# Kernel optimization log

Hardware: AMD Instinct MI355X
Metric: run time of the kernel (lower is better)

Reference implementation:

```python
import jax, jax.numpy as jnp
import numpy as np

B, T_D, T_P = 64, 256, 1024
DRUG_DIM, PROT_DIM, D = 128, 128, 128
MAX_LEN = 1024
NEG = -1e9


def _linear_params(k, out_d, in_d):
    k1, k2 = jax.random.split(k)
    lim = 1.0 / np.sqrt(in_d)
    W = jax.random.uniform(k1, (out_d, in_d), minval=-lim, maxval=lim, dtype=jnp.float32)
    b = jax.random.uniform(k2, (out_d,), minval=-lim, maxval=lim, dtype=jnp.float32)
    return W, b


def setup_inputs() -> dict:
    key = jax.random.key(0)
    ks = jax.random.split(key, 13)
    inp = {
        'smiles_embeddings': jax.random.normal(ks[0], (B, T_D, DRUG_DIM), dtype=jnp.float32),
        'protein_embeddings': jax.random.normal(ks[1], (B, T_P, PROT_DIM), dtype=jnp.float32),
        'smiles_mask': jax.random.randint(ks[2], (B, T_D), 0, 2, dtype=jnp.int32),
        'protein_mask': jax.random.randint(ks[3], (B, T_P), 0, 2, dtype=jnp.int32),
        # torch inits pos_bias to zeros; small random values make the test nontrivial
        'pos_bias': 0.02 * jax.random.normal(ks[4], (MAX_LEN, MAX_LEN), dtype=jnp.float32),
    }
    names = [('Wqd', 'bqd', DRUG_DIM), ('Wkp', 'bkp', PROT_DIM), ('Wvp', 'bvp', PROT_DIM),
             ('Wqp', 'bqp', PROT_DIM), ('Wkd', 'bkd', DRUG_DIM), ('Wvd', 'bvd', DRUG_DIM),
             ('Wpd', 'bpd', D), ('Wpp', 'bpp', D)]
    for i, (wn, bn, in_d) in enumerate(names):
        W, b = _linear_params(ks[5 + i], D, in_d)
        inp[wn] = W
        inp[bn] = b
    return inp


def _lin(x, W, b):
    return x @ W.T + b


def _aft(q, k, v, pb_masked, Wp, bp):
    # q: [B,Ti,D]; k,v: [B,Tj,D]; pb_masked: [B,Ti,Tj]
    max_k = k.max(axis=1, keepdims=True)              # per (b,d) over seq j
    max_pb = pb_masked.max(axis=2, keepdims=True)     # per (b,i) over j
    exp_k = jnp.exp(k - max_k)                        # [B,Tj,D]
    exp_pb = jnp.exp(pb_masked - max_pb)              # [B,Ti,Tj]
    num = jnp.einsum('bij,bjd->bid', exp_pb, exp_k * v)
    den = jnp.einsum('bij,bjd->bid', exp_pb, exp_k)
    y = jax.nn.sigmoid(q) * num / den
    return _lin(y, Wp, bp)


def reference(smiles_embeddings, protein_embeddings, smiles_mask, protein_mask, pos_bias,
              Wqd, bqd, Wkp, bkp, Wvp, bvp, Wqp, bqp, Wkd, bkd, Wvd, bvd, Wpd, bpd, Wpp, bpp):
    Td = smiles_embeddings.shape[1]
    Tp = protein_embeddings.shape[1]
    combined = smiles_mask[:, :, None] * protein_mask[:, None, :]  # [B,Td,Tp]
    pb = pos_bias[:Td, :Tp][None]                                   # [1,Td,Tp]

    # drug queries attend over protein keys/values
    pb_d = jnp.where(combined == 0, NEG, pb)
    y_d = _aft(_lin(smiles_embeddings, Wqd, bqd),
               _lin(protein_embeddings, Wkp, bkp),
               _lin(protein_embeddings, Wvp, bvp), pb_d, Wpd, bpd)

    # protein queries attend over drug keys/values (transposed pos bias)
    pb_p = jnp.where(jnp.swapaxes(combined, 1, 2) == 0, NEG, jnp.swapaxes(pb, 1, 2))
    y_p = _aft(_lin(protein_embeddings, Wqp, bqp),
               _lin(smiles_embeddings, Wkd, bkd),
               _lin(smiles_embeddings, Wvd, bvd), pb_p, Wpp, bpp)

    y_d = jnp.where(smiles_mask[:, :, None] == 0, NEG, y_d).max(axis=1)   # [B,D]
    y_p = jnp.where(protein_mask[:, :, None] == 0, NEG, y_p).max(axis=1)  # [B,D]
    return y_d, y_p
```

## Files before the change

### kernel.cpp

```cpp
#include <hip/hip_runtime.h>
#include <cstdint>
#include <cstddef>

#define NEGV -1e9f

typedef __bf16 bf16x8 __attribute__((ext_vector_type(8)));
typedef float f32x4 __attribute__((ext_vector_type(4)));
typedef unsigned short us4 __attribute__((ext_vector_type(4)));
typedef unsigned short us8 __attribute__((ext_vector_type(8)));

__device__ __forceinline__ unsigned short f2bf(float f) {
  unsigned int u = __float_as_uint(f);
  u += 0x7fffu + ((u >> 16) & 1u);
  return (unsigned short)(u >> 16);
}
__device__ __forceinline__ float bf2f(unsigned short u) {
  return __uint_as_float(((unsigned)u) << 16);
}


__global__ void prep_kernel(const float* __restrict__ w0, const float* __restrict__ w1,
                            const float* __restrict__ w2, const float* __restrict__ w3,
                            const float* __restrict__ w4, const float* __restrict__ w5,
                            const float* __restrict__ w6, const float* __restrict__ w7,
                            unsigned short* __restrict__ Wbf,
                            const float* __restrict__ pb,
                            unsigned short* __restrict__ epb,
                            unsigned short* __restrict__ epbT,
                            unsigned int* __restrict__ outEnc) {
  __shared__ unsigned short t[32][33];
  const int blk = blockIdx.x, tid = threadIdx.x;
  if (blk < 64) {
    outEnc[blk * 256 + tid] = 0u;
    return;
  }
  if (blk < 192) {
    const float* Ws[8] = {w0, w1, w2, w3, w4, w5, w6, w7};
    int idx = (blk - 64) * 256 + tid;
    int mat = idx >> 12, off = idx & 4095;
    float4 v = *(const float4*)&Ws[mat][(size_t)off * 4];
    us4 p;
    p.x = f2bf(v.x); p.y = f2bf(v.y); p.z = f2bf(v.z); p.w = f2bf(v.w);
    *(us4*)&Wbf[(size_t)mat * 16384 + (size_t)off * 4] = p;
    return;
  }
  const int bid = blk - 192;
  const int j0 = (bid & 31) * 32, i0 = (bid >> 5) * 32;
  const int tx = tid & 31, ty = tid >> 5;
#pragma unroll
  for (int r = 0; r < 4; ++r) {
    int i = i0 + ty + r * 8;
    unsigned short u = f2bf(__expf(pb[(size_t)i * 1024 + j0 + tx]));
    epb[(size_t)i * 1024 + j0 + tx] = u;
    t[ty + r * 8][tx] = u;
  }
  __syncthreads();
#pragma unroll
  for (int r = 0; r < 4; ++r)
    epbT[(size_t)(j0 + ty + r * 8) * 256 + i0 + tx] = t[tx][ty + r * 8];
}

__global__ __launch_bounds__(512, 4) void proj3_all(
    const float* __restrict__ smiles, const float* __restrict__ prot,
    const int* __restrict__ smask, const int* __restrict__ pmask,
    const unsigned short* __restrict__ Wbf,
    const float* __restrict__ bqd, const float* __restrict__ bkd, const float* __restrict__ bvd,
    const float* __restrict__ bqp, const float* __restrict__ bkp, const float* __restrict__ bvp,
    const unsigned short* __restrict__ epb, const unsigned short* __restrict__ epbT,
    unsigned short* __restrict__ AFd, unsigned short* __restrict__ AFp,
    unsigned short* __restrict__ SQd, unsigned short* __restrict__ BKd,
    unsigned short* __restrict__ BVd,
    unsigned short* __restrict__ SQp, unsigned short* __restrict__ BKp,
    unsigned short* __restrict__ BVp) {
  const int tid = threadIdx.x;

  if (blockIdx.x >= 1280) {
    int sid = (blockIdx.x - 1280) * 512 + tid;
    if (sid < 32768) {
      int lane = sid & 63, kt = (sid >> 6) & 31, it = sid >> 11;
      int i = it * 16 + (lane & 15), j = kt * 32 + (lane >> 4) * 8;
      *(us8*)&AFd[(size_t)sid * 8] = *(const us8*)&epb[(size_t)i * 1024 + j];
    } else {
      int s2 = sid - 32768;
      int lane = s2 & 63, kt = (s2 >> 6) & 7, it = s2 >> 9;
      int i = it * 16 + (lane & 15), j = kt * 32 + (lane >> 4) * 8;
      *(us8*)&AFp[(size_t)s2 * 8] = *(const us8*)&epbT[(size_t)i * 256 + j];
    }
    return;
  }

  __shared__ unsigned short xL[64 * 136];

  const float* X; const int* mask;
  const unsigned short *Wq, *Wk, *Wv;
  const float *bq, *bk_, *bv;
  unsigned short *SQ, *BK, *BV;
  int T, g0;
  if (blockIdx.x < 256) {
    X = smiles; mask = smask; T = 256; g0 = blockIdx.x * 64;
    Wq = Wbf; Wk = Wbf + 16384; Wv = Wbf + 32768;
    bq = bqd; bk_ = bkd; bv = bvd;
    SQ = SQd; BK = BKd; BV = BVd;
  } else {
    X = prot; mask = pmask; T = 1024; g0 = (blockIdx.x - 256) * 64;
    Wq = Wbf + 3 * 16384; Wk = Wbf + 4 * 16384; Wv = Wbf + 5 * 16384;
    bq = bqp; bk_ = bkp; bv = bvp;
    SQ = SQp; BK = BKp; BV = BVp;
  }
  const int b = g0 / T;
  const int tl0 = g0 - b * T;
  const int NIT = T / 16, NKT = T / 32;

#pragma unroll
  for (int r = 0; r < 4; ++r) {
    int i4 = tid + 512 * r;
    int t = i4 >> 5, k4 = (i4 & 31) * 4;
    float4 v = *(const float4*)&X[(size_t)(g0 + t) * 128 + k4];
    us4 p;
    p.x = f2bf(v.x); p.y = f2bf(v.y); p.z = f2bf(v.z); p.w = f2bf(v.w);
    *(us4*)&xL[t * 136 + k4] = p;
  }
  __syncthreads();

  const int lane = tid & 63, wave = tid >> 6;
  const int lo = lane & 15, hi = lane >> 4;

  if (wave < 4) {
    const int d0 = wave * 32;
    f32x4 aK[4][2], aV[4][2];
#pragma unroll
    for (int a = 0; a < 4; ++a)
#pragma unroll
      for (int s = 0; s < 2; ++s)
#pragma unroll
        for (int r = 0; r < 4; ++r) { aK[a][s][r] = 0.f; aV[a][s][r] = 0.f; }

#pragma unroll
    for (int kt = 0; kt < 128; kt += 32) {
      bf16x8 bK[2], bV[2];
#pragma unroll
      for (int s = 0; s < 2; ++s) {
        size_t roff = (size_t)(d0 + s * 16 + lo) * 128 + kt + hi * 8;
        bK[s] = *(const bf16x8*)&Wk[roff];
        bV[s] = *(const bf16x8*)&Wv[roff];
      }
#pragma unroll
      for (int a = 0; a < 4; ++a) {
        bf16x8 af = *(const bf16x8*)&xL[(a * 16 + lo) * 136 + kt + hi * 8];
#pragma unroll
        for (int s = 0; s < 2; ++s) {
          aK[a][s] = __builtin_amdgcn_mfma_f32_16x16x32_bf16(af, bK[s], aK[a][s], 0, 0, 0);
          aV[a][s] = __builtin_amdgcn_mfma_f32_16x16x32_bf16(af, bV[s], aV[a][s], 0, 0, 0);
        }
      }
    }

#pragma unroll
    for (int s = 0; s < 2; ++s) {
      int dt = (d0 >> 4) + s;
      float bbk = bk_[d0 + s * 16 + lo], bbv = bv[d0 + s * 16 + lo];
#pragma unroll
      for (int a = 0; a < 4; ++a) {
        int kt = (tl0 >> 5) + (a >> 1);
        int lane_f = ((a & 1) * 2 + (hi >> 1)) * 16 + lo;
        us4 vk, vv;
#pragma unroll
        for (int r = 0; r < 4; ++r) {
          int tg = g0 + a * 16 + hi * 4 + r;
          int mk = mask[tg];
          float ek = mk ? __expf(aK[a][s][r] + bbk) : 0.f;
          float ekv = ek * (aV[a][s][r] + bbv);
          vk[r] = f2bf(ek);
          vv[r] = f2bf(ekv);
        }
        size_t q4 = ((((size_t)b * NKT + kt) * 8 + dt) * 64 + lane_f) * 2 + (hi & 1);
        ((us4*)BK)[q4] = vk;
        ((us4*)BV)[q4] = vv;
      }
    }
  } else {
    const int d0 = (wave - 4) * 32;
    f32x4 aQ[4][2];
#pragma unroll
    for (int a = 0; a < 4; ++a)
#pragma unroll
      for (int s = 0; s < 2; ++s)
#pragma unroll
        for (int r = 0; r < 4; ++r) aQ[a][s][r] = 0.f;

#pragma unroll
    for (int kt = 0; kt < 128; kt += 32) {
      bf16x8 bQ[2];
#pragma unroll
      for (int s = 0; s < 2; ++s) {
        size_t roff = (size_t)(d0 + s * 16 + lo) * 128 + kt + hi * 8;
        bQ[s] = *(const bf16x8*)&Wq[roff];
      }
#pragma unroll
      for (int a = 0; a < 4; ++a) {
        bf16x8 af = *(const bf16x8*)&xL[(a * 16 + lo) * 136 + kt + hi * 8];
#pragma unroll
        for (int s = 0; s < 2; ++s)
          aQ[a][s] = __builtin_amdgcn_mfma_f32_16x16x32_bf16(af, bQ[s], aQ[a][s], 0, 0, 0);
      }
    }

#pragma unroll
    for (int s = 0; s < 2; ++s) {
      int dt = (d0 >> 4) + s;
      float bb = bq[d0 + s * 16 + lo];
#pragma unroll
      for (int a = 0; a < 4; ++a) {
        int it = (tl0 >> 4) + a;
        us4 v;
#pragma unroll
        for (int r = 0; r < 4; ++r) {
          float q = aQ[a][s][r] + bb;
          v[r] = f2bf(1.f / (1.f + __expf(-q)));
        }
        ((us4*)SQ)[(((size_t)b * NIT + it) * 8 + dt) * 64 + lane] = v;
      }
    }
  }
}

__global__ __launch_bounds__(512, 4) void aft_all(
    const unsigned short* __restrict__ AFd, const unsigned short* __restrict__ AFp,
    const unsigned short* __restrict__ SQd, const unsigned short* __restrict__ BKd,
    const unsigned short* __restrict__ BVd,
    const unsigned short* __restrict__ SQp, const unsigned short* __restrict__ BKp,
    const unsigned short* __restrict__ BVp,
    const int* __restrict__ smask, const int* __restrict__ pmask,
    const unsigned short* __restrict__ Wbf,
    const float* __restrict__ bpd, const float* __restrict__ bpp,
    unsigned int* __restrict__ outEnc) {
  __shared__ unsigned short smem[16384 + 128 * 136];
  unsigned short* denL = smem;
  unsigned short* yL = smem + 16384;

  const int blk = blockIdx.x;
  const unsigned short *AF, *BK, *BV, *SQ, *Wp;
  const float* bp;
  const int* msk;
  unsigned int* oEnc;
  int b, i0, NKT, NIT;
  if (blk < 128) {
    b = blk & 63; i0 = (blk >> 6) * 128; NKT = 32; NIT = 16;
    AF = AFd; BK = BKp; BV = BVp; SQ = SQd;
    Wp = Wbf + 6 * 16384; bp = bpd; msk = smask + b * 256 + i0; oEnc = outEnc;
  } else {
    int k = blk - 128;
    b = k & 63; i0 = (k >> 6) * 128; NKT = 8; NIT = 64;
    AF = AFp; BK = BKd; BV = BVd; SQ = SQp;
    Wp = Wbf + 7 * 16384; bp = bpp; msk = pmask + b * 1024 + i0; oEnc = outEnc + 8192;
  }

  const int tid = threadIdx.x, lane = tid & 63, w = tid >> 6;
  const int lo = lane & 15, hi = lane >> 4;
  const int wv = w & 3;
  const int wi = (wv >> 1) * 64, wd = (wv & 1) * 64;
  const int it0 = (i0 + wi) >> 4;
  const int dt0 = wd >> 4;

  const unsigned short* Bb = ((w < 4) ? BV : BK) + (size_t)b * NKT * 8 * 64 * 8;

  f32x4 acc[4][4];
#pragma unroll
  for (int a = 0; a < 4; ++a)
#pragma unroll
    for (int n = 0; n < 4; ++n)
#pragma unroll
      for (int r = 0; r < 4; ++r) acc[a][n][r] = 0.f;

#pragma unroll 2
  for (int kt = 0; kt < NKT; ++kt) {
    bf16x8 af[4];
#pragma unroll
    for (int a = 0; a < 4; ++a)
      af[a] = *(const bf16x8*)&AF[(((size_t)(it0 + a) * NKT + kt) * 64 + lane) * 8];
    bf16x8 bb[4];
#pragma unroll
    for (int n = 0; n < 4; ++n)
      bb[n] = *(const bf16x8*)&Bb[(((size_t)kt * 8 + dt0 + n) * 64 + lane) * 8];
#pragma unroll
    for (int a = 0; a < 4; ++a)
#pragma unroll
      for (int n = 0; n < 4; ++n)
        acc[a][n] = __builtin_amdgcn_mfma_f32_16x16x32_bf16(af[a], bb[n], acc[a][n], 0, 0, 0);
  }

  if (w >= 4) {
#pragma unroll
    for (int a = 0; a < 4; ++a)
#pragma unroll
      for (int n = 0; n < 4; ++n) {
        us4 v;
#pragma unroll
        for (int r = 0; r < 4; ++r) v[r] = f2bf(acc[a][n][r]);
        ((us4*)denL)[(wv * 16 + a * 4 + n) * 64 + lane] = v;
      }
  }
  __syncthreads();

  if (w < 4) {
#pragma unroll
    for (int a = 0; a < 4; ++a)
#pragma unroll
      for (int n = 0; n < 4; ++n) {
        us4 dv = ((const us4*)denL)[(wv * 16 + a * 4 + n) * 64 + lane];
        us4 q = ((const us4*)SQ)[(((size_t)b * NIT + it0 + a) * 8 + dt0 + n) * 64 + lane];
        int iL = wi + a * 16 + hi * 4;
        int d = wd + n * 16 + lo;
#pragma unroll
        for (int r = 0; r < 4; ++r) {
          float y = bf2f(q[r]) * __fdividef(acc[a][n][r], bf2f(dv[r]));
          yL[(iL + r) * 136 + d] = f2bf(y);
        }
      }
  }
  __syncthreads();

  const int wi2 = (w & 3) * 32, wd2 = (w >> 2) * 64;
  f32x4 aZ[2][4];
#pragma unroll
  for (int a = 0; a < 2; ++a)
#pragma unroll
    for (int n = 0; n < 4; ++n)
#pragma unroll
      for (int r = 0; r < 4; ++r) aZ[a][n][r] = 0.f;

#pragma unroll
  for (int kt = 0; kt < 128; kt += 32) {
    bf16x8 bw[4];
#pragma unroll
    for (int n = 0; n < 4; ++n)
      bw[n] = *(const bf16x8*)&Wp[(size_t)(wd2 + n * 16 + lo) * 128 + kt + hi * 8];
#pragma unroll
    for (int a = 0; a < 2; ++a) {
      bf16x8 af = *(const bf16x8*)&yL[(wi2 + a * 16 + lo) * 136 + kt + hi * 8];
#pragma unroll
      for (int n = 0; n < 4; ++n)
        aZ[a][n] = __builtin_amdgcn_mfma_f32_16x16x32_bf16(af, bw[n], aZ[a][n], 0, 0, 0);
    }
  }

#pragma unroll
  for (int n = 0; n < 4; ++n) {
    int d = wd2 + n * 16 + lo;
    float bb = bp[d];
    float m = NEGV;
#pragma unroll
    for (int a = 0; a < 2; ++a)
#pragma unroll
      for (int r = 0; r < 4; ++r) {
        int iL = wi2 + a * 16 + hi * 4 + r;
        float z = aZ[a][n][r] + bb;
        m = msk[iL] ? fmaxf(m, z) : m;
      }
    m = fmaxf(m, __shfl_xor(m, 16, 64));
    m = fmaxf(m, __shfl_xor(m, 32, 64));
    if (hi == 0) {
      unsigned bits = __float_as_uint(m);
      unsigned key = (bits & 0x80000000u) ? ~bits : (bits | 0x80000000u);
      atomicMax(&oEnc[b * 128 + d], key);
    }
  }
}

__global__ void out_decode(unsigned int* o) {
  int i = blockIdx.x * 256 + threadIdx.x;
  unsigned k = o[i];
  unsigned bits = (k & 0x80000000u) ? (k ^ 0x80000000u) : ~k;
  ((float*)o)[i] = __uint_as_float(bits);
}

extern "C" void kernel_launch(void* const* d_in, const int* in_sizes, int n_in,
                              void* d_out, int out_size, void* d_ws, size_t ws_size,
                              hipStream_t stream) {
  const float* smiles = (const float*)d_in[0];
  const float* prot   = (const float*)d_in[1];
  const int* smask = (const int*)d_in[2];
  const int* pmask = (const int*)d_in[3];
  const float* pos_bias = (const float*)d_in[4];
  const float* Wqd = (const float*)d_in[5];  const float* bqd = (const float*)d_in[6];
  const float* Wkp = (const float*)d_in[7];  const float* bkp = (const float*)d_in[8];
  const float* Wvp = (const float*)d_in[9];  const float* bvp = (const float*)d_in[10];
  const float* Wqp = (const float*)d_in[11]; const float* bqp = (const float*)d_in[12];
  const float* Wkd = (const float*)d_in[13]; const float* bkd = (const float*)d_in[14];
  const float* Wvd = (const float*)d_in[15]; const float* bvd = (const float*)d_in[16];
  const float* Wpd = (const float*)d_in[17]; const float* bpd = (const float*)d_in[18];
  const float* Wpp = (const float*)d_in[19]; const float* bpp = (const float*)d_in[20];

  unsigned short* u = (unsigned short*)d_ws;
  unsigned short* BKp_  = u;
  unsigned short* BVp_  = BKp_ + 8388608;
  unsigned short* BKd_  = BVp_ + 8388608;
  unsigned short* BVd_  = BKd_ + 2097152;
  unsigned short* SQd_  = BVd_ + 2097152;
  unsigned short* SQp_  = SQd_ + 2097152;
  unsigned short* epb_  = SQp_ + 8388608;
  unsigned short* epbT_ = epb_ + 262144;
  unsigned short* AFd_  = epbT_ + 262144;
  unsigned short* AFp_  = AFd_ + 262144;
  unsigned short* Wbf   = AFp_ + 262144;

  prep_kernel<<<448, 256, 0, stream>>>(Wqd, Wkd, Wvd, Wqp, Wkp, Wvp, Wpd, Wpp,
                                       Wbf, pos_bias, epb_, epbT_,
                                       (unsigned int*)d_out);

  proj3_all<<<1408, 512, 0, stream>>>(smiles, prot, smask, pmask, Wbf,
                                      bqd, bkd, bvd, bqp, bkp, bvp,
                                      epb_, epbT_, AFd_, AFp_,
                                      SQd_, BKd_, BVd_, SQp_, BKp_, BVp_);

  aft_all<<<640, 512, 0, stream>>>(AFd_, AFp_, SQd_, BKd_, BVd_,
                                   SQp_, BKp_, BVp_, smask, pmask, Wbf,
                                   bpd, bpp, (unsigned int*)d_out);

  out_decode<<<64, 256, 0, stream>>>((unsigned int*)d_out);
}
```

Baseline: 190.1 us.

## Merge Q/K/V projection waves into 256-thread blocks and pack bf16 conversions

The projection kernel moves from 512-thread blocks, where four waves computed K/V and four computed Q, to 256-thread blocks where each wave computes Q, K and V for its 32-column slice. The aim is to balance MFMA work evenly across waves and reuse each LDS A-fragment load for three products instead of two. The shuffle tail is re-gridded to match (1536 blocks of 256). Separately, manual float-to-bf16 rounding is replaced by the packed __float22bfloat162_rn intrinsic in several places. More accumulators per wave (24 f32x4) raise register pressure, and the launch-bounds occupancy hint is dropped.

```diff
diff --git a/kernel.cpp b/kernel.cpp
--- a/kernel.cpp
+++ b/kernel.cpp
@@ -1,4 +1,5 @@
 #include <hip/hip_runtime.h>
+#include <hip/hip_bf16.h>
 #include <cstdint>
 #include <cstddef>
 
@@ -16,6 +17,18 @@
 }
 __device__ __forceinline__ float bf2f(unsigned short u) {
   return __uint_as_float(((unsigned)u) << 16);
+}
+__device__ __forceinline__ unsigned int f2bf2(float a, float b) {
+  __hip_bfloat162 h = __float22bfloat162_rn(make_float2(a, b));
+  unsigned int u;
+  __builtin_memcpy(&u, &h, 4);
+  return u;
+}
+__device__ __forceinline__ us4 pk4(float a, float b, float c, float d) {
+  uint2 u = make_uint2(f2bf2(a, b), f2bf2(c, d));
+  us4 r;
+  __builtin_memcpy(&r, &u, 8);
+  return r;
 }
 
 
@@ -39,9 +52,7 @@
     int idx = (blk - 64) * 256 + tid;
     int mat = idx >> 12, off = idx & 4095;
     float4 v = *(const float4*)&Ws[mat][(size_t)off * 4];
-    us4 p;
-    p.x = f2bf(v.x); p.y = f2bf(v.y); p.z = f2bf(v.z); p.w = f2bf(v.w);
-    *(us4*)&Wbf[(size_t)mat * 16384 + (size_t)off * 4] = p;
+    *(us4*)&Wbf[(size_t)mat * 16384 + (size_t)off * 4] = pk4(v.x, v.y, v.z, v.w);
     return;
   }
   const int bid = blk - 192;
@@ -60,7 +71,7 @@
     epbT[(size_t)(j0 + ty + r * 8) * 256 + i0 + tx] = t[tx][ty + r * 8];
 }
 
-__global__ __launch_bounds__(512, 4) void proj3_all(
+__global__ __launch_bounds__(256) void proj3_all(
     const float* __restrict__ smiles, const float* __restrict__ prot,
     const int* __restrict__ smask, const int* __restrict__ pmask,
     const unsigned short* __restrict__ Wbf,
@@ -75,7 +86,7 @@
   const int tid = threadIdx.x;
 
   if (blockIdx.x >= 1280) {
-    int sid = (blockIdx.x - 1280) * 512 + tid;
+    int sid = (blockIdx.x - 1280) * 256 + tid;
     if (sid < 32768) {
       int lane = sid & 63, kt = (sid >> 6) & 31, it = sid >> 11;
       int i = it * 16 + (lane & 15), j = kt * 32 + (lane >> 4) * 8;
@@ -112,114 +123,82 @@
   const int NIT = T / 16, NKT = T / 32;
 
 #pragma unroll
-  for (int r = 0; r < 4; ++r) {
-    int i4 = tid + 512 * r;
+  for (int r = 0; r < 8; ++r) {
+    int i4 = tid + 256 * r;
     int t = i4 >> 5, k4 = (i4 & 31) * 4;
     float4 v = *(const float4*)&X[(size_t)(g0 + t) * 128 + k4];
-    us4 p;
-    p.x = f2bf(v.x); p.y = f2bf(v.y); p.z = f2bf(v.z); p.w = f2bf(v.w);
-    *(us4*)&xL[t * 136 + k4] = p;
+    *(us4*)&xL[t * 136 + k4] = pk4(v.x, v.y, v.z, v.w);
   }
   __syncthreads();
 
   const int lane = tid & 63, wave = tid >> 6;
   const int lo = lane & 15, hi = lane >> 4;
-
-  if (wave < 4) {
-    const int d0 = wave * 32;
-    f32x4 aK[4][2], aV[4][2];
-#pragma unroll
-    for (int a = 0; a < 4; ++a)
-#pragma unroll
-      for (int s = 0; s < 2; ++s)
-#pragma unroll
-        for (int r = 0; r < 4; ++r) { aK[a][s][r] = 0.f; aV[a][s][r] = 0.f; }
-
-#pragma unroll
-    for (int kt = 0; kt < 128; kt += 32) {
-      bf16x8 bK[2], bV[2];
+  const int d0 = wave * 32;
+
+  f32x4 aQ[4][2], aK[4][2], aV[4][2];
+#pragma unroll
+  for (int a = 0; a < 4; ++a)
+#pragma unroll
+    for (int s = 0; s < 2; ++s)
+#pragma unroll
+      for (int r = 0; r < 4; ++r) { aQ[a][s][r] = 0.f; aK[a][s][r] = 0.f; aV[a][s][r] = 0.f; }
+
+#pragma unroll
+  for (int kt = 0; kt < 128; kt += 32) {
+    bf16x8 bQ[2], bK[2], bV[2];
+#pragma unroll
+    for (int s = 0; s < 2; ++s) {
+      size_t roff = (size_t)(d0 + s * 16 + lo) * 128 + kt + hi * 8;
+      bQ[s] = *(const bf16x8*)&Wq[roff];
+      bK[s] = *(const bf16x8*)&Wk[roff];
+      bV[s] = *(const bf16x8*)&Wv[roff];
+    }
+#pragma unroll
+    for (int a = 0; a < 4; ++a) {
+      bf16x8 af = *(const bf16x8*)&xL[(a * 16 + lo) * 136 + kt + hi * 8];
 #pragma unroll
       for (int s = 0; s < 2; ++s) {
-        size_t roff = (size_t)(d0 + s * 16 + lo) * 128 + kt + hi * 8;
-        bK[s] = *(const bf16x8*)&Wk[roff];
-        bV[s] = *(const bf16x8*)&Wv[roff];
+        aQ[a][s] = __builtin_amdgcn_mfma_f32_16x16x32_bf16(af, bQ[s], aQ[a][s], 0, 0, 0);
+        aK[a][s] = __builtin_amdgcn_mfma_f32_16x16x32_bf16(af, bK[s], aK[a][s], 0, 0, 0);
+        aV[a][s] = __builtin_amdgcn_mfma_f32_16x16x32_bf16(af, bV[s], aV[a][s], 0, 0, 0);
       }
-#pragma unroll
-      for (int a = 0; a < 4; ++a) {
-        bf16x8 af = *(const bf16x8*)&xL[(a * 16 + lo) * 136 + kt + hi * 8];
-#pragma unroll
-        for (int s = 0; s < 2; ++s) {
-          aK[a][s] = __builtin_amdgcn_mfma_f32_16x16x32_bf16(af, bK[s], aK[a][s], 0, 0, 0);
-          aV[a][s] = __builtin_amdgcn_mfma_f32_16x16x32_bf16(af, bV[s], aV[a][s], 0, 0, 0);
-        }
+    }
+  }
+
+#pragma unroll
+  for (int s = 0; s < 2; ++s) {
+    int dt = (d0 >> 4) + s;
+    float bb = bq[d0 + s * 16 + lo];
+#pragma unroll
+    for (int a = 0; a < 4; ++a) {
+      int it = (tl0 >> 4) + a;
+      float y0 = 1.f / (1.f + __expf(-(aQ[a][s][0] + bb)));
+      float y1 = 1.f / (1.f + __expf(-(aQ[a][s][1] + bb)));
+      float y2 = 1.f / (1.f + __expf(-(aQ[a][s][2] + bb)));
+      float y3 = 1.f / (1.f + __expf(-(aQ[a][s][3] + bb)));
+      ((us4*)SQ)[(((size_t)b * NIT + it) * 8 + dt) * 64 + lane] = pk4(y0, y1, y2, y3);
+    }
+  }
+
+#pragma unroll
+  for (int s = 0; s < 2; ++s) {
+    int dt = (d0 >> 4) + s;
+    float bbk = bk_[d0 + s * 16 + lo], bbv = bv[d0 + s * 16 + lo];
+#pragma unroll
+    for (int a = 0; a < 4; ++a) {
+      int kt = (tl0 >> 5) + (a >> 1);
+      int lane_f = ((a & 1) * 2 + (hi >> 1)) * 16 + lo;
+      float ek[4], ekv[4];
+#pragma unroll
+      for (int r = 0; r < 4; ++r) {
+        int tg = g0 + a * 16 + hi * 4 + r;
+        int mk = mask[tg];
+        ek[r] = mk ? __expf(aK[a][s][r] + bbk) : 0.f;
+        ekv[r] = ek[r] * (aV[a][s][r] + bbv);
       }
-    }
-
-#pragma unroll
-    for (int s = 0; s < 2; ++s) {
-      int dt = (d0 >> 4) + s;
-      float bbk = bk_[d0 + s * 16 + lo], bbv = bv[d0 + s * 16 + lo];
-#pragma unroll
-      for (int a = 0; a < 4; ++a) {
-        int kt = (tl0 >> 5) + (a >> 1);
-        int lane_f = ((a & 1) * 2 + (hi >> 1)) * 16 + lo;
-        us4 vk, vv;
-#pragma unroll
-        for (int r = 0; r < 4; ++r) {
-          int tg = g0 + a * 16 + hi * 4 + r;
-          int mk = mask[tg];
-          float ek = mk ? __expf(aK[a][s][r] + bbk) : 0.f;
-          float ekv = ek * (aV[a][s][r] + bbv);
-          vk[r] = f2bf(ek);
-          vv[r] = f2bf(ekv);
-        }
-        size_t q4 = ((((size_t)b * NKT + kt) * 8 + dt) * 64 + lane_f) * 2 + (hi & 1);
-        ((us4*)BK)[q4] = vk;
-        ((us4*)BV)[q4] = vv;
-      }
-    }
-  } else {
-    const int d0 = (wave - 4) * 32;
-    f32x4 aQ[4][2];
-#pragma unroll
-    for (int a = 0; a < 4; ++a)
-#pragma unroll
-      for (int s = 0; s < 2; ++s)
-#pragma unroll
-        for (int r = 0; r < 4; ++r) aQ[a][s][r] = 0.f;
-
-#pragma unroll
-    for (int kt = 0; kt < 128; kt += 32) {
-      bf16x8 bQ[2];
-#pragma unroll
-      for (int s = 0; s < 2; ++s) {
-        size_t roff = (size_t)(d0 + s * 16 + lo) * 128 + kt + hi * 8;
-        bQ[s] = *(const bf16x8*)&Wq[roff];
-      }
-#pragma unroll
-      for (int a = 0; a < 4; ++a) {
-        bf16x8 af = *(const bf16x8*)&xL[(a * 16 + lo) * 136 + kt + hi * 8];
-#pragma unroll
-        for (int s = 0; s < 2; ++s)
-          aQ[a][s] = __builtin_amdgcn_mfma_f32_16x16x32_bf16(af, bQ[s], aQ[a][s], 0, 0, 0);
-      }
-    }
-
-#pragma unroll
-    for (int s = 0; s < 2; ++s) {
-      int dt = (d0 >> 4) + s;
-      float bb = bq[d0 + s * 16 + lo];
-#pragma unroll
-      for (int a = 0; a < 4; ++a) {
-        int it = (tl0 >> 4) + a;
-        us4 v;
-#pragma unroll
-        for (int r = 0; r < 4; ++r) {
-          float q = aQ[a][s][r] + bb;
-          v[r] = f2bf(1.f / (1.f + __expf(-q)));
-        }
-        ((us4*)SQ)[(((size_t)b * NIT + it) * 8 + dt) * 64 + lane] = v;
-      }
+      size_t q4 = ((((size_t)b * NKT + kt) * 8 + dt) * 64 + lane_f) * 2 + (hi & 1);
+      ((us4*)BK)[q4] = pk4(ek[0], ek[1], ek[2], ek[3]);
+      ((us4*)BV)[q4] = pk4(ekv[0], ekv[1], ekv[2], ekv[3]);
     }
   }
 }
@@ -293,12 +272,9 @@
 #pragma unroll
     for (int a = 0; a < 4; ++a)
 #pragma unroll
-      for (int n = 0; n < 4; ++n) {
-        us4 v;
-#pragma unroll
-        for (int r = 0; r < 4; ++r) v[r] = f2bf(acc[a][n][r]);
-        ((us4*)denL)[(wv * 16 + a * 4 + n) * 64 + lane] = v;
-      }
+      for (int n = 0; n < 4; ++n)
+        ((us4*)denL)[(wv * 16 + a * 4 + n) * 64 + lane] =
+            pk4(acc[a][n][0], acc[a][n][1], acc[a][n][2], acc[a][n][3]);
   }
   __syncthreads();
 
@@ -408,7 +384,7 @@
                                        Wbf, pos_bias, epb_, epbT_,
                                        (unsigned int*)d_out);
 
-  proj3_all<<<1408, 512, 0, stream>>>(smiles, prot, smask, pmask, Wbf,
+  proj3_all<<<1536, 256, 0, stream>>>(smiles, prot, smask, pmask, Wbf,
                                       bqd, bkd, bvd, bqp, bkp, bvp,
                                       epb_, epbT_, AFd_, AFp_,
                                       SQd_, BKd_, BVd_, SQp_, BKp_, BVp_);
```

New measurement: 187.5 us. Within noise of the previous version (-1.4%).
